# Optimization experiments

Measured on AMD Instinct MI355X. Metric: run time of the kernel, lower is better.

## Reference

```python
import jax, jax.numpy as jnp
import numpy as np

SUN = 9.0          # sudoku digit range constant (SuN in the repo)
N_HEAD = 8
D_MODEL = 128
CHUNK = 24         # query-chunk size for memory-efficient L1 distance (744 = 31*24)


def _qgelu(z):
    return z * jax.nn.sigmoid(1.702 * z)


def _l1_scores(q, k, scale):
    """a[b,s,d,h] = -sum_w |q[b,s,h,w] - k[b,d,h,w]| * scale, computed in query chunks
    to avoid the full [b,n,n,h,w] broadcast intermediate (mirrors the L1Attn CUDA kernel)."""
    b, n, h, w = q.shape
    nc = n // CHUNK
    qc = q.reshape(b, nc, CHUNK, h, w).transpose(1, 0, 2, 3, 4)  # [nc,b,c,h,w]

    def f(qi):
        # qi: [b,c,h,w] -> scores [b,c,n,h]
        return -jnp.abs(qi[:, :, None, :, :] - k[:, None, :, :, :]).sum(-1) * scale

    a = jax.lax.map(f, qc)                                        # [nc,b,c,n,h]
    return a.transpose(1, 0, 2, 3, 4).reshape(b, n, n, h)


def _forward(x, wk, wqv_w, wqv_b, fanin_w, fanin_b):
    b, n, w = x.shape
    h = N_HEAD
    # wqv: Linear(d_model -> 3*n_head*d_model), split into q, vf, vb
    v = (x @ wqv_w.T + wqv_b).reshape(b, n, 3 * h, w)
    q, vf, vb = v[:, :, :h, :], v[:, :, h:2 * h, :], v[:, :, 2 * h:, :]
    # k = x broadcast to heads, scaled by learned per-head wk
    k = x[:, :, None, :] * wk[None, None, :, :]                   # [b,n,h,w]

    # dense branch: L1 attention with an extra zero "null" logit, softmax over source dim
    a = _l1_scores(q, k, 1.0 / np.sqrt(w))                        # [b,s,d,h]
    a = jnp.concatenate([a, jnp.zeros((b, 1, n, h), a.dtype)], axis=1)  # zero row at s=n
    a = jax.nn.softmax(a, axis=1)[:, :n]                          # [b,s,d,h]

    # bidirectional value combine: forward (vf) and backward (vb)
    bf = jnp.einsum('bsdh,bshw->bdhw', a, vf)
    bb = jnp.einsum('bdsh,bshw->bdhw', a, vb)
    y = (bf + bb).sum(axis=2)                                     # sum over heads -> [b,n,w]

    y = _qgelu(y + SUN / 2.0) - SUN / 2.0
    y = y @ fanin_w.T + fanin_b
    return x + y


def setup_inputs() -> dict:
    key = jax.random.key(0)
    k0, k1, k2 = jax.random.split(key, 3)
    b, n = 4, 744  # ntok NOT a multiple of 16 (code asserts padn > 0)
    x = jax.random.normal(k0, (b, n, D_MODEL), jnp.float32)
    wk = 0.005 * jnp.ones((N_HEAD, D_MODEL), jnp.float32)
    wqv_w = 0.005 * jax.random.normal(k1, (3 * N_HEAD * D_MODEL, D_MODEL), jnp.float32)
    wqv_b = jnp.zeros((3 * N_HEAD * D_MODEL,), jnp.float32)
    fanin_w = 0.005 * jax.random.normal(k2, (D_MODEL, D_MODEL), jnp.float32)
    fanin_b = jnp.zeros((D_MODEL,), jnp.float32)
    return {"x": x, "wk": wk, "wqv_w": wqv_w, "wqv_b": wqv_b,
            "fanin_w": fanin_w, "fanin_b": fanin_b, "layer": 0, "pas": 0}


def reference(x, wk, wqv_w, wqv_b, fanin_w, fanin_b, layer, pas):
    # hcoo = ['dense'] is hardcoded; layer/pas select the (single) dense branch.
    return _forward(x, wk, wqv_w, wqv_b, fanin_w, fanin_b)
```

## Files before the change

### kernel.cpp

```cpp
#include <hip/hip_runtime.h>
#include <hip/hip_bf16.h>
#include <cstdint>

#define N_TOK 744
#define NP    768
#define DW    128
#define NH    8

typedef __attribute__((ext_vector_type(4))) float f32x4;
typedef __attribute__((ext_vector_type(4))) unsigned int u32x4;
typedef __attribute__((ext_vector_type(8))) __bf16 bf16x8;
typedef __attribute__((ext_vector_type(4))) __bf16 bf16x4;

__device__ __forceinline__ unsigned int sadu8(unsigned int a, unsigned int b, unsigned int c) {
    unsigned int d;
    asm("v_sad_u8 %0, %1, %2, %3" : "=v"(d) : "v"(a), "v"(b), "v"(c));
    return d;
}

__global__ void k_zinit(float* Z, int n) {
    int i = blockIdx.x * 256 + threadIdx.x;
    if (i < n) Z[i] = 1.0f;
}

__global__ __launch_bounds__(256) void k_cvt(
    const float* __restrict__ x, const float* __restrict__ wqv_w,
    __bf16* __restrict__ xb, __bf16* __restrict__ wb, int M, int Mp)
{
    int t = blockIdx.x * 256 + threadIdx.x;
    int xgroups = Mp * 32;
    if (t < xgroups) {
        int r = t >> 5, c4 = (t & 31) * 4;
        f32x4 v = {};
        if (r < M) v = *(const f32x4*)(x + (size_t)r * DW + c4);
        bf16x4 o;
        #pragma unroll
        for (int i = 0; i < 4; i++) o[i] = (__bf16)v[i];
        *(bf16x4*)&xb[(size_t)r * DW + c4] = o;
    } else if (t < xgroups + 3072 * 32) {
        int t2 = t - xgroups;
        int r = t2 >> 5, c4 = (t2 & 31) * 4;
        f32x4 v = *(const f32x4*)(wqv_w + (size_t)r * DW + c4);
        bf16x4 o;
        #pragma unroll
        for (int i = 0; i < 4; i++) o[i] = (__bf16)v[i];
        *(bf16x4*)&wb[(size_t)r * DW + c4] = o;
    }
}

__global__ __launch_bounds__(256) void k_proj(
    const __bf16* __restrict__ xb, const __bf16* __restrict__ wb,
    const float* __restrict__ wqv_b,
    float* __restrict__ qbuf, __bf16* __restrict__ vf_t, __bf16* __restrict__ vb_t,
    int M)
{
    __shared__ __align__(16) char smem[65536];
    int bx = blockIdx.x, by = blockIdx.y;
    int tid = threadIdx.x, l = tid & 63, wv = tid >> 6;
    int lr = l & 15, lg = l >> 4;
    bool vpath = (bx >= 8);

    const char* xg = (const char*)xb + (size_t)by * 128 * 256;
    const char* wg = (const char*)wb + (size_t)bx * 128 * 256;

    #pragma unroll
    for (int u = wv; u < 64; u += 4) {
        int row = 4 * (u & 31) + (l >> 4);
        unsigned int chunk = (unsigned int)(l & 15) ^ (unsigned int)(row & 7);
        const char* gp = (u < 32 ? xg : wg) + (size_t)row * 256 + chunk * 16;
        char* lp = &smem[u * 1024];
        __builtin_amdgcn_global_load_lds(
            (const __attribute__((address_space(1))) void*)gp,
            (__attribute__((address_space(3))) void*)lp, 16, 0, 0);
    }
    asm volatile("s_waitcnt vmcnt(0)" ::: "memory");
    __builtin_amdgcn_s_barrier();

    const char* Xt = smem;
    const char* Wt = smem + 32768;
    const char* TA = vpath ? Wt : Xt;
    const char* TB = vpath ? Xt : Wt;

    f32x4 acc[2][8] = {};
    #pragma unroll
    for (int kk = 0; kk < 4; kk++) {
        int cA = kk * 4 + lg;
        bf16x8 a[2];
        #pragma unroll
        for (int mr = 0; mr < 2; mr++) {
            int row = wv * 32 + mr * 16 + lr;
            a[mr] = *(const bf16x8*)(TA + row * 256 + (cA ^ (row & 7)) * 16);
        }
        #pragma unroll
        for (int nc = 0; nc < 8; nc++) {
            int row = nc * 16 + lr;
            bf16x8 bfr = *(const bf16x8*)(TB + row * 256 + (cA ^ (row & 7)) * 16);
            acc[0][nc] = __builtin_amdgcn_mfma_f32_16x16x32_bf16(a[0], bfr, acc[0][nc], 0, 0, 0);
            acc[1][nc] = __builtin_amdgcn_mfma_f32_16x16x32_bf16(a[1], bfr, acc[1][nc], 0, 0, 0);
        }
    }

    if (!vpath) {
        int hd = bx;
        #pragma unroll
        for (int nc = 0; nc < 8; nc++) {
            int wi = nc * 16 + lr;
            float bias = wqv_b[bx * 128 + wi];
            #pragma unroll
            for (int mr = 0; mr < 2; mr++)
                #pragma unroll
                for (int j = 0; j < 4; j++) {
                    int r = by * 128 + wv * 32 + mr * 16 + lg * 4 + j;
                    if (r >= M) continue;
                    int b = r / N_TOK, s = r % N_TOK;
                    qbuf[(((size_t)b * NH + hd) * NP + s) * DW + wi] = acc[mr][nc][j] + bias;
                }
        }
    } else {
        __bf16* dst0 = (bx < 16) ? vf_t : vb_t;
        int hh = (bx < 16) ? (bx - 8) : (bx - 16);
        #pragma unroll
        for (int mr = 0; mr < 2; mr++)
            #pragma unroll
            for (int j = 0; j < 4; j++) {
                int wi = wv * 32 + mr * 16 + lg * 4 + j;
                float bias = wqv_b[bx * 128 + wi];
                #pragma unroll
                for (int nc = 0; nc < 8; nc++) {
                    int r = by * 128 + nc * 16 + lr;
                    if (r >= M) continue;
                    int b = r / N_TOK, st = r % N_TOK;
                    dst0[(((size_t)b * NH + hh) * DW + wi) * NP + st] =
                        (__bf16)(acc[mr][nc][j] + bias);
                }
            }
    }
}

__global__ __launch_bounds__(256) void k_scores(
    const float* __restrict__ qbuf, const float* __restrict__ x,
    const float* __restrict__ wk,
    __bf16* __restrict__ e1, __bf16* __restrict__ e2, float* __restrict__ Z)
{
    __shared__ unsigned int qt[32][132];
    __shared__ unsigned int kt[32][132];
    int bh = blockIdx.z; int b = bh >> 3, h = bh & 7;
    int s0 = blockIdx.y * 128, d0 = blockIdx.x * 128;
    int tid = threadIdx.x;
    int ty = tid >> 4, tx = tid & 15;
    const float* qbase = qbuf + (size_t)bh * NP * DW;
    const float* xbase = x + (size_t)b * N_TOK * DW;
    const float* wkh = wk + h * DW;

    int cg = tid & 31;
    int r0 = tid >> 5;
    float w4[4];
    *(f32x4*)w4 = *(const f32x4*)(wkh + 4 * cg);
    const float CL = 0.9921875f;
    #pragma unroll
    for (int pass = 0; pass < 16; pass++) {
        int r = pass * 8 + r0;
        f32x4 qv4 = *(const f32x4*)(qbase + (size_t)(s0 + r) * DW + 4 * cg);
        unsigned int uq = 0;
        #pragma unroll
        for (int e = 0; e < 4; e++) {
            float v = fminf(fmaxf(qv4[e], -CL), CL);
            unsigned int u = (unsigned int)__builtin_fmaf(v, 128.0f, 128.5f);
            uq |= u << (8 * e);
        }
        qt[cg][r] = uq;
        int d = d0 + r;
        f32x4 xv4 = {};
        if (d < N_TOK) xv4 = *(const f32x4*)(xbase + (size_t)d * DW + 4 * cg);
        unsigned int uk = 0;
        #pragma unroll
        for (int e = 0; e < 4; e++) {
            float v = fminf(fmaxf(xv4[e] * w4[e], -CL), CL);
            unsigned int u = (unsigned int)__builtin_fmaf(v, 128.0f, 128.5f);
            uk |= u << (8 * e);
        }
        kt[cg][r] = uk;
    }
    __syncthreads();

    unsigned int acc[8][8] = {};
    #pragma unroll 4
    for (int g = 0; g < 32; g++) {
        unsigned int qv[8], kv[8];
        *(u32x4*)&qv[0] = *(const u32x4*)&qt[g][ty * 8];
        *(u32x4*)&qv[4] = *(const u32x4*)&qt[g][ty * 8 + 4];
        *(u32x4*)&kv[0] = *(const u32x4*)&kt[g][tx * 8];
        *(u32x4*)&kv[4] = *(const u32x4*)&kt[g][tx * 8 + 4];
        #pragma unroll
        for (int i = 0; i < 8; i++)
            #pragma unroll
            for (int j = 0; j < 8; j++)
                acc[i][j] = sadu8(qv[i], kv[j], acc[i][j]);
    }

    const float SS = 0.08838834764831845f / 128.0f;
    float e[8][8]; float colsum[8] = {};
    int sb = s0 + ty * 8, db = d0 + tx * 8;
    #pragma unroll
    for (int i = 0; i < 8; i++)
        #pragma unroll
        for (int j = 0; j < 8; j++) {
            float ev = ((sb + i) < N_TOK && (db + j) < N_TOK)
                       ? __expf(-(float)acc[i][j] * SS) : 0.0f;
            e[i][j] = ev; colsum[j] += ev;
        }
    size_t ebase = (size_t)bh * NP * NP;
    #pragma unroll
    for (int i = 0; i < 8; i++) {
        bf16x8 v;
        #pragma unroll
        for (int j = 0; j < 8; j++) v[j] = (__bf16)e[i][j];
        *(bf16x8*)&e2[ebase + (size_t)(sb + i) * NP + db] = v;
    }
    #pragma unroll
    for (int j = 0; j < 8; j++) {
        bf16x8 v;
        #pragma unroll
        for (int i = 0; i < 8; i++) v[i] = (__bf16)e[i][j];
        *(bf16x8*)&e1[ebase + (size_t)(db + j) * NP + sb] = v;
    }
    __syncthreads();
    float* red = (float*)&qt[0][0];
    #pragma unroll
    for (int j = 0; j < 8; j++) red[ty * 128 + tx * 8 + j] = colsum[j];
    __syncthreads();
    if (tid < 128) {
        float z = 0;
        #pragma unroll
        for (int r = 0; r < 16; r++) z += red[r * 128 + tid];
        atomicAdd(&Z[(size_t)bh * NP + d0 + tid], z);
    }
}

__global__ void k_scalevb(__bf16* vb_t, const float* __restrict__ Z, long total8)
{
    long idx = (long)blockIdx.x * blockDim.x + threadIdx.x;
    if (idx >= total8) return;
    size_t base = (size_t)idx * 8;
    int s = (int)(base % NP);
    int bh = (int)((base / NP) / DW);
    bf16x8 v = *(bf16x8*)&vb_t[base];
    const float* Zp = Z + (size_t)bh * NP + s;
    bf16x8 o;
    #pragma unroll
    for (int i = 0; i < 8; i++) o[i] = (__bf16)((float)v[i] / Zp[i]);
    *(bf16x8*)&vb_t[base] = o;
}

__global__ __launch_bounds__(256) void k_apply(
    const __bf16* __restrict__ e1, const __bf16* __restrict__ e2,
    const __bf16* __restrict__ vf_t, const __bf16* __restrict__ vb_t,
    const float* __restrict__ Z, __bf16* __restrict__ y0f, __bf16* __restrict__ y0b)
{
    __shared__ __align__(16) char smem[2][40960];
    int bh = blockIdx.y;
    int tid = threadIdx.x;
    int l = tid & 63, wv = tid >> 6;
    int lr = l & 15, lg = l >> 4;
    int m0b = blockIdx.x * 32;
    int m0 = m0b + (wv & 1) * 16;
    bool doF = (wv < 2);

    const char* e1b = (const char*)e1 + 2 * ((size_t)bh * NP * NP + (size_t)m0b * NP);
    const char* e2b = (const char*)e2 + 2 * ((size_t)bh * NP * NP + (size_t)m0b * NP);
    const char* vfb = (const char*)vf_t + 2 * ((size_t)bh * DW * NP);
    const char* vbb = (const char*)vb_t + 2 * ((size_t)bh * DW * NP);
    unsigned int swz = (16u * (l & 7)) ^ (((unsigned)(l >> 3)) << 4);
    size_t rowoff = (size_t)(l >> 3) * (NP * 2);

    #define STAGE(bi, kk) do {                                                        \
        for (int u = wv; u < 40; u += 4) {                                            \
            char* lp = &smem[bi][u * 1024];                                           \
            const char* gp;                                                           \
            if (u < 4)       gp = e1b + (size_t)(8 * u) * (NP * 2);                   \
            else if (u < 8)  gp = e2b + (size_t)(8 * (u - 4)) * (NP * 2);             \
            else if (u < 24) gp = vfb + (size_t)(8 * (u - 8)) * (NP * 2);             \
            else             gp = vbb + (size_t)(8 * (u - 24)) * (NP * 2);            \
            gp += rowoff + (size_t)(kk) * 2 + swz;                                    \
            __builtin_amdgcn_global_load_lds(                                         \
                (const __attribute__((address_space(1))) void*)gp,                    \
                (__attribute__((address_space(3))) void*)lp, 16, 0, 0);               \
        }                                                                             \
    } while (0)

    const char* eL0 = &smem[0][doF ? 0 : 4096];
    const char* vL0 = &smem[0][doF ? 8192 : 24576];
    int mloc = (wv & 1) * 16 + lr;
    unsigned int rswz = ((unsigned)(lr & 7)) << 4;

    f32x4 acc[8] = {};
    STAGE(0, 0);
    STAGE(1, 64);
    for (int t = 0; t < 12; t++) {
        if (t < 11) asm volatile("s_waitcnt vmcnt(10)" ::: "memory");
        else        asm volatile("s_waitcnt vmcnt(0)" ::: "memory");
        __builtin_amdgcn_s_barrier();
        const char* eL = eL0 + (t & 1) * 40960;
        const char* vL = vL0 + (t & 1) * 40960;
        #pragma unroll
        for (int ph = 0; ph < 2; ph++) {
            unsigned int csw = (ph * 64 + lg * 16) ^ rswz;
            bf16x8 a = *(const bf16x8*)(eL + mloc * 128 + csw);
            #pragma unroll
            for (int ct = 0; ct < 8; ct++) {
                bf16x8 bfr = *(const bf16x8*)(vL + (ct * 16 + lr) * 128 + csw);
                acc[ct] = __builtin_amdgcn_mfma_f32_16x16x32_bf16(a, bfr, acc[ct], 0, 0, 0);
            }
        }
        __builtin_amdgcn_s_barrier();
        if (t + 2 < 12) STAGE(t & 1, (t + 2) * 64);
    }
    #undef STAGE

    float sc[4];
    #pragma unroll
    for (int j = 0; j < 4; j++)
        sc[j] = doF ? (1.0f / Z[(size_t)bh * NP + m0 + lg * 4 + j]) : 1.0f;
    __bf16* yb = (doF ? y0f : y0b) + ((size_t)bh * NP + m0) * DW;
    #pragma unroll
    for (int ct = 0; ct < 8; ct++)
        #pragma unroll
        for (int j = 0; j < 4; j++)
            yb[(size_t)(lg * 4 + j) * DW + ct * 16 + lr] = (__bf16)(sc[j] * acc[ct][j]);
}

__global__ __launch_bounds__(256) void k_fin1(
    const __bf16* __restrict__ y0f, const __bf16* __restrict__ y0b,
    __bf16* __restrict__ g, int M)
{
    int idx = blockIdx.x * 256 + threadIdx.x;
    int r = idx >> 4;
    int c = (idx & 15) * 8;
    if (r >= M) return;
    int b = r / N_TOK, s = r % N_TOK;
    float sum[8] = {};
    size_t base = ((size_t)b * NH * NP + s) * DW + c;
    #pragma unroll
    for (int h = 0; h < NH; h++) {
        bf16x8 vf_ = *(const bf16x8*)&y0f[base + (size_t)h * NP * DW];
        bf16x8 vb_ = *(const bf16x8*)&y0b[base + (size_t)h * NP * DW];
        #pragma unroll
        for (int i = 0; i < 8; i++) sum[i] += (float)vf_[i] + (float)vb_[i];
    }
    bf16x8 o;
    #pragma unroll
    for (int i = 0; i < 8; i++) {
        float z = sum[i] + 4.5f;
        float gv = z / (1.0f + __expf(-1.702f * z)) - 4.5f;
        o[i] = (__bf16)gv;
    }
    *(bf16x8*)&g[(size_t)r * DW + c] = o;
}

__global__ __launch_bounds__(256) void k_fin2(
    const __bf16* __restrict__ g, const float* __restrict__ x,
    const float* __restrict__ fanin_w, const float* __restrict__ fanin_b,
    float* __restrict__ out, int M)
{
    int tid = threadIdx.x;
    int l = tid & 63, wv = tid >> 6;
    int lr = l & 15, lg = l >> 4;
    int m0 = blockIdx.x * 64 + wv * 16;
    f32x4 acc[8] = {};
    int ar = m0 + lr; if (ar >= M) ar = M - 1;
    const __bf16* gp = g + (size_t)ar * DW;
    for (int kk = 0; kk < 128; kk += 32) {
        int ko = kk + lg * 8;
        bf16x8 a = *(const bf16x8*)(gp + ko);
        #pragma unroll
        for (int ct = 0; ct < 8; ct++) {
            const float* wp = fanin_w + (size_t)(ct * 16 + lr) * DW + ko;
            float w0[8];
            *(f32x4*)w0 = *(const f32x4*)wp; *(f32x4*)(w0 + 4) = *(const f32x4*)(wp + 4);
            bf16x8 bfr;
            #pragma unroll
            for (int j2 = 0; j2 < 8; j2++) bfr[j2] = (__bf16)w0[j2];
            acc[ct] = __builtin_amdgcn_mfma_f32_16x16x32_bf16(a, bfr, acc[ct], 0, 0, 0);
        }
    }
    #pragma unroll
    for (int ct = 0; ct < 8; ct++) {
        int c = ct * 16 + lr;
        float fb = fanin_b[c];
        #pragma unroll
        for (int j = 0; j < 4; j++) {
            int r = m0 + lg * 4 + j;
            if (r < M) out[(size_t)r * DW + c] = x[(size_t)r * DW + c] + acc[ct][j] + fb;
        }
    }
}

extern "C" void kernel_launch(void* const* d_in, const int* in_sizes, int n_in,
                              void* d_out, int out_size, void* d_ws, size_t ws_size,
                              hipStream_t stream)
{
    const float* x       = (const float*)d_in[0];
    const float* wk      = (const float*)d_in[1];
    const float* wqv_w   = (const float*)d_in[2];
    const float* wqv_b   = (const float*)d_in[3];
    const float* fanin_w = (const float*)d_in[4];
    const float* fanin_b = (const float*)d_in[5];
    int B = in_sizes[0] / (N_TOK * DW);
    int M = B * N_TOK;
    int Mp = ((M + 127) / 128) * 128;

    char* ws = (char*)d_ws;
    size_t off = 0;
    float*  qbuf = (float*)(ws + off);  off += (size_t)B * NH * NP * DW * 4;
    __bf16* vf_t = (__bf16*)(ws + off); off += (size_t)B * NH * DW * NP * 2;
    __bf16* vb_t = (__bf16*)(ws + off); off += (size_t)B * NH * DW * NP * 2;
    __bf16* e1   = (__bf16*)(ws + off); off += (size_t)B * NH * NP * NP * 2;
    __bf16* e2   = (__bf16*)(ws + off); off += (size_t)B * NH * NP * NP * 2;
    float*  Z    = (float*)(ws + off);  off += (size_t)B * NH * NP * 4;
    __bf16* y0b  = (__bf16*)(ws + off); off += (size_t)B * NH * NP * DW * 2;
    __bf16* xb   = (__bf16*)(ws + off); off += (size_t)Mp * DW * 2;
    __bf16* wb   = (__bf16*)(ws + off); off += (size_t)3072 * DW * 2;
    if (off > ws_size) return;
    __bf16* y0f = (__bf16*)qbuf;
    __bf16* g   = vf_t;

    int zn = B * NH * NP;
    k_zinit<<<(zn + 255) / 256, 256, 0, stream>>>(Z, zn);

    int cvt_threads = (Mp + 3072) * 32;
    k_cvt<<<(cvt_threads + 255) / 256, 256, 0, stream>>>(x, wqv_w, xb, wb, M, Mp);

    dim3 gp(24, Mp / 128);
    k_proj<<<gp, 256, 0, stream>>>(xb, wb, wqv_b, qbuf, vf_t, vb_t, M);

    dim3 gs(NP / 128, NP / 128, B * NH);
    k_scores<<<gs, 256, 0, stream>>>(qbuf, x, wk, e1, e2, Z);

    long total8 = (long)B * NH * DW * NP / 8;
    k_scalevb<<<(int)((total8 + 255) / 256), 256, 0, stream>>>(vb_t, Z, total8);

    dim3 ga(NP / 32, B * NH);
    k_apply<<<ga, 256, 0, stream>>>(e1, e2, vf_t, vb_t, Z, y0f, y0b);

    int f1blocks = (M * (DW / 8) + 255) / 256;
    k_fin1<<<f1blocks, 256, 0, stream>>>(y0f, y0b, g, M);

    k_fin2<<<(M + 63) / 64, 256, 0, stream>>>(g, x, fanin_w, fanin_b, (float*)d_out, M);
}
```

Before: 211.3 us.

## Precompute u8-quantized Q/K in a separate kernel and re-layout K tile in LDS

Adds a k_quant kernel that clamps and quantizes q and wk-scaled x into packed u8 buffers once per (batch, head, row), so k_scores no longer reloads fp32 rows and repeats the quantization for every 128x128 tile. k_scores now loads the packed rows directly and writes K into a split, padded shared-memory layout meant to reduce bank conflicts in the SAD inner loop. This adds one kernel launch and an extra global round trip through the new workspace buffers.

```diff
diff --git a/kernel.cpp b/kernel.cpp
--- a/kernel.cpp
+++ b/kernel.cpp
@@ -137,60 +137,86 @@
     }
 }
 
-__global__ __launch_bounds__(256) void k_scores(
+__global__ __launch_bounds__(256) void k_quant(
     const float* __restrict__ qbuf, const float* __restrict__ x,
     const float* __restrict__ wk,
+    unsigned int* __restrict__ qu8, unsigned int* __restrict__ ku8, int B)
+{
+    int t = blockIdx.x * 256 + threadIdx.x;
+    int c8 = t & 7;
+    int rr = t >> 3;
+    int row = rr % NP;
+    int bh = rr / NP;
+    if (bh >= B * NH) return;
+    int b = bh >> 3, h = bh & 7;
+    bool valid = row < N_TOK;
+    int w0 = c8 * 16;
+    const float* qp = qbuf + ((size_t)bh * NP + row) * DW + w0;
+    const float* xp = x + ((size_t)b * N_TOK + (valid ? row : 0)) * DW + w0;
+    const float* wp = wk + h * DW + w0;
+    const float CL = 0.9921875f;
+    unsigned int outq[4], outk[4];
+    #pragma unroll
+    for (int u = 0; u < 4; u++) {
+        f32x4 qv = {}, xv = {};
+        if (valid) { qv = *(const f32x4*)(qp + u * 4); xv = *(const f32x4*)(xp + u * 4); }
+        f32x4 wv = *(const f32x4*)(wp + u * 4);
+        unsigned int pq = 0, pk = 0;
+        #pragma unroll
+        for (int e = 0; e < 4; e++) {
+            float a = fminf(fmaxf(qv[e], -CL), CL);
+            pq |= ((unsigned int)__builtin_fmaf(a, 128.0f, 128.5f)) << (8 * e);
+            float c = fminf(fmaxf(xv[e] * wv[e], -CL), CL);
+            pk |= ((unsigned int)__builtin_fmaf(c, 128.0f, 128.5f)) << (8 * e);
+        }
+        outq[u] = pq; outk[u] = pk;
+    }
+    size_t dst = ((size_t)bh * NP + row) * 32 + c8 * 4;
+    *(u32x4*)&qu8[dst] = *(u32x4*)outq;
+    *(u32x4*)&ku8[dst] = *(u32x4*)outk;
+}
+
+__global__ __launch_bounds__(256) void k_scores(
+    const unsigned int* __restrict__ qu8, const unsigned int* __restrict__ ku8,
     __bf16* __restrict__ e1, __bf16* __restrict__ e2, float* __restrict__ Z)
 {
-    __shared__ unsigned int qt[32][132];
-    __shared__ unsigned int kt[32][132];
-    int bh = blockIdx.z; int b = bh >> 3, h = bh & 7;
+    __shared__ __align__(16) unsigned int qt[32][132];
+    __shared__ __align__(16) unsigned int kts[2 * 2176 + 4];
+    int bh = blockIdx.z;
     int s0 = blockIdx.y * 128, d0 = blockIdx.x * 128;
     int tid = threadIdx.x;
     int ty = tid >> 4, tx = tid & 15;
-    const float* qbase = qbuf + (size_t)bh * NP * DW;
-    const float* xbase = x + (size_t)b * N_TOK * DW;
-    const float* wkh = wk + h * DW;
-
-    int cg = tid & 31;
-    int r0 = tid >> 5;
-    float w4[4];
-    *(f32x4*)w4 = *(const f32x4*)(wkh + 4 * cg);
-    const float CL = 0.9921875f;
-    #pragma unroll
-    for (int pass = 0; pass < 16; pass++) {
-        int r = pass * 8 + r0;
-        f32x4 qv4 = *(const f32x4*)(qbase + (size_t)(s0 + r) * DW + 4 * cg);
-        unsigned int uq = 0;
-        #pragma unroll
-        for (int e = 0; e < 4; e++) {
-            float v = fminf(fmaxf(qv4[e], -CL), CL);
-            unsigned int u = (unsigned int)__builtin_fmaf(v, 128.0f, 128.5f);
-            uq |= u << (8 * e);
-        }
-        qt[cg][r] = uq;
-        int d = d0 + r;
-        f32x4 xv4 = {};
-        if (d < N_TOK) xv4 = *(const f32x4*)(xbase + (size_t)d * DW + 4 * cg);
-        unsigned int uk = 0;
-        #pragma unroll
-        for (int e = 0; e < 4; e++) {
-            float v = fminf(fmaxf(xv4[e] * w4[e], -CL), CL);
-            unsigned int u = (unsigned int)__builtin_fmaf(v, 128.0f, 128.5f);
-            uk |= u << (8 * e);
-        }
-        kt[cg][r] = uk;
+
+    {
+        int row = tid & 127;
+        bool isq = tid < 128;
+        const unsigned int* src = isq
+            ? qu8 + ((size_t)bh * NP + s0 + row) * 32
+            : ku8 + ((size_t)bh * NP + d0 + row) * 32;
+        unsigned int buf[32];
+        #pragma unroll
+        for (int c = 0; c < 8; c++)
+            *(u32x4*)&buf[c * 4] = *(const u32x4*)(src + c * 4);
+        if (isq) {
+            #pragma unroll
+            for (int i = 0; i < 32; i++) qt[i][row] = buf[i];
+        } else {
+            unsigned int* dst = (row < 64) ? &kts[row] : &kts[2180 + (row - 64)];
+            #pragma unroll
+            for (int i = 0; i < 32; i++) dst[i * 68] = buf[i];
+        }
     }
     __syncthreads();
 
+    const char* kbase = (const char*)((tx < 8) ? &kts[tx * 8] : &kts[2180 + (tx - 8) * 8]);
     unsigned int acc[8][8] = {};
     #pragma unroll 4
     for (int g = 0; g < 32; g++) {
         unsigned int qv[8], kv[8];
         *(u32x4*)&qv[0] = *(const u32x4*)&qt[g][ty * 8];
         *(u32x4*)&qv[4] = *(const u32x4*)&qt[g][ty * 8 + 4];
-        *(u32x4*)&kv[0] = *(const u32x4*)&kt[g][tx * 8];
-        *(u32x4*)&kv[4] = *(const u32x4*)&kt[g][tx * 8 + 4];
+        *(u32x4*)&kv[0] = *(const u32x4*)(kbase + g * 272);
+        *(u32x4*)&kv[4] = *(const u32x4*)(kbase + g * 272 + 16);
         #pragma unroll
         for (int i = 0; i < 8; i++)
             #pragma unroll
@@ -420,6 +446,8 @@
     __bf16* y0b  = (__bf16*)(ws + off); off += (size_t)B * NH * NP * DW * 2;
     __bf16* xb   = (__bf16*)(ws + off); off += (size_t)Mp * DW * 2;
     __bf16* wb   = (__bf16*)(ws + off); off += (size_t)3072 * DW * 2;
+    unsigned int* qu8 = (unsigned int*)(ws + off); off += (size_t)B * NH * NP * 32 * 4;
+    unsigned int* ku8 = (unsigned int*)(ws + off); off += (size_t)B * NH * NP * 32 * 4;
     if (off > ws_size) return;
     __bf16* y0f = (__bf16*)qbuf;
     __bf16* g   = vf_t;
@@ -433,8 +461,11 @@
     dim3 gp(24, Mp / 128);
     k_proj<<<gp, 256, 0, stream>>>(xb, wb, wqv_b, qbuf, vf_t, vb_t, M);
 
+    int qthreads = B * NH * NP * 8;
+    k_quant<<<(qthreads + 255) / 256, 256, 0, stream>>>(qbuf, x, wk, qu8, ku8, B);
+
     dim3 gs(NP / 128, NP / 128, B * NH);
-    k_scores<<<gs, 256, 0, stream>>>(qbuf, x, wk, e1, e2, Z);
+    k_scores<<<gs, 256, 0, stream>>>(qu8, ku8, e1, e2, Z);
 
     long total8 = (long)B * NH * DW * NP / 8;
     k_scalevb<<<(int)((total8 + 255) / 256), 256, 0, stream>>>(vb_t, Z, total8);
```

Result: faster. 205.1 us (-2.9%).
